# Optimization experiments

Measured on AMD Instinct MI355X. Metric: run time of the kernel, lower is better.

The kernel has to match this reference:

```python
import jax, jax.numpy as jnp
import numpy as np

REL_DIM = 1024
NUM_HEADS = 16
HEAD_DIM = REL_DIM // NUM_HEADS
REL_EMB_DIM = 256
B, K = 32, 512
SCALE = 1.0 / float(np.sqrt(HEAD_DIM))


def setup_inputs() -> dict:
    key = jax.random.key(0)
    ks = jax.random.split(key, 7)
    s = 1.0 / float(np.sqrt(REL_DIM))
    return {
        "h_R": jax.random.normal(ks[0], (B, K, REL_DIM), dtype=jnp.float32),
        "R": jax.random.normal(ks[1], (K, REL_EMB_DIM), dtype=jnp.float32),
        "W_q": jax.random.normal(ks[2], (REL_DIM, REL_DIM), dtype=jnp.float32) * s,
        "W_k": jax.random.normal(ks[3], (REL_DIM, REL_DIM), dtype=jnp.float32) * s,
        "W_v": jax.random.normal(ks[4], (REL_DIM, REL_DIM), dtype=jnp.float32) * s,
        "W_o": jax.random.normal(ks[5], (REL_DIM, REL_DIM), dtype=jnp.float32) * s,
        "w_sim": jax.random.normal(ks[6], (NUM_HEADS,), dtype=jnp.float32) * 0.1,
    }


def reference(h_R, R, W_q, W_k, W_v, W_o, w_sim):
    Bb, Kk, _ = h_R.shape
    H, D = NUM_HEADS, HEAD_DIM
    # torch Linear: x @ W.T ; then split heads -> (B, H, K, D)
    def proj(x, W):
        return jnp.einsum('bkd,ed->bke', x, W).reshape(Bb, Kk, H, D).transpose(0, 2, 1, 3)
    q = proj(h_R, W_q)
    k = proj(h_R, W_k)
    v = proj(h_R, W_v)
    attn = jnp.einsum('bhqd,bhkd->bhqk', q, k) * SCALE
    # cosine-similarity bias (batch-independent): (H, K, K)
    R_norm = R / jnp.maximum(jnp.linalg.norm(R, axis=-1, keepdims=True), 1e-12)
    sim = R_norm @ R_norm.T  # (K, K)
    bias = w_sim[:, None, None] * sim[None]  # (H, K, K)
    attn = attn + bias[None]
    alpha = jax.nn.softmax(attn, axis=-1)
    out = jnp.einsum('bhqk,bhkd->bhqd', alpha, v)
    out = out.transpose(0, 2, 1, 3).reshape(Bb, Kk, H * D)
    return jnp.einsum('bkd,ed->bke', out, W_o)
```

## Files before the change

### kernel.cpp

```cpp
#include <hip/hip_runtime.h>

#define SEQK 512
#define NH 16
#define HD 64
#define RD 1024
#define BBATCH 32
#define QK_SCALE 0.125f

typedef unsigned short u16;
using bf16x8 = __attribute__((ext_vector_type(8))) short;
using f32x4  = __attribute__((ext_vector_type(4))) float;

__device__ __forceinline__ u16 f2bf(float f) {
  unsigned u = __float_as_uint(f);
  u += 0x7FFFu + ((u >> 16) & 1u);
  return (u16)(u >> 16);
}
__device__ __forceinline__ float bf2f(u16 v) {
  return __uint_as_float(((unsigned)v) << 16);
}

__device__ __forceinline__ void async_cp16(const void* g, void* l) {
  __builtin_amdgcn_global_load_lds(
      (__attribute__((address_space(1))) void*)(void*)g,
      (__attribute__((address_space(3))) void*)l,
      16, 0, 0);
}

__global__ void convert_kernel(const float* __restrict__ hR,
                               const float* __restrict__ Wq, const float* __restrict__ Wk,
                               const float* __restrict__ Wv, const float* __restrict__ Wo,
                               u16* __restrict__ hR16,
                               u16* __restrict__ Wq16, u16* __restrict__ Wk16,
                               u16* __restrict__ Wv16, u16* __restrict__ Wo16) {
  size_t i4 = (size_t)blockIdx.x * blockDim.x + threadIdx.x;
  size_t e = i4 * 4;
  const float* src; u16* dst; size_t off;
  if (e < 16777216u) { src = hR; dst = hR16; off = e; }
  else {
    size_t r = e - 16777216u;
    int w = (int)(r >> 20);
    off = r & 1048575u;
    src = (w == 0 ? Wq : w == 1 ? Wk : w == 2 ? Wv : Wo);
    dst = (w == 0 ? Wq16 : w == 1 ? Wk16 : w == 2 ? Wv16 : Wo16);
  }
  float4 v = *(const float4*)(src + off);
  ushort4 o;
  o.x = f2bf(v.x); o.y = f2bf(v.y); o.z = f2bf(v.z); o.w = f2bf(v.w);
  *(ushort4*)(dst + off) = o;
}

__global__ void rnorm_kernel(const float* __restrict__ R, float* __restrict__ Rn) {
  int row = blockIdx.x;
  int lane = threadIdx.x;
  float4 v = *(const float4*)(R + (size_t)row * 256 + lane * 4);
  float ss = v.x * v.x + v.y * v.y + v.z * v.z + v.w * v.w;
  for (int off = 32; off; off >>= 1) ss += __shfl_xor(ss, off);
  float s = 1.0f / fmaxf(sqrtf(ss), 1e-12f);
  float4 o = {v.x * s, v.y * s, v.z * s, v.w * s};
  *(float4*)(Rn + (size_t)row * 256 + lane * 4) = o;
}

__global__ void sim_kernel(const float* __restrict__ Rn, u16* __restrict__ sim16) {
  __shared__ float Rl[16 * 256];
  int i0 = blockIdx.x * 16;
  int t = threadIdx.x;
  #pragma unroll
  for (int i = 0; i < 4; i++) {
    int f = t + i * 256;
    *(float4*)&Rl[f * 4] = *(const float4*)(Rn + (size_t)i0 * 256 + f * 4);
  }
  __syncthreads();
  for (int jj = 0; jj < 2; jj++) {
    int j = jj * 256 + t;
    float acc[16];
    #pragma unroll
    for (int i = 0; i < 16; i++) acc[i] = 0.f;
    for (int c = 0; c < 64; c++) {
      float4 rv = *(const float4*)(Rn + (size_t)j * 256 + c * 4);
      #pragma unroll
      for (int i = 0; i < 16; i++) {
        float4 a = *(const float4*)&Rl[i * 256 + c * 4];
        acc[i] += a.x * rv.x + a.y * rv.y + a.z * rv.z + a.w * rv.w;
      }
    }
    #pragma unroll
    for (int i = 0; i < 16; i++) sim16[(size_t)(i0 + i) * 512 + j] = f2bf(acc[i]);
  }
}

template <int MODE>
__global__ __launch_bounds__(256)
void gemm_kernel(const u16* __restrict__ A,
                 const u16* __restrict__ B0, const u16* __restrict__ B1,
                 const u16* __restrict__ B2,
                 u16* __restrict__ q16, u16* __restrict__ k16, u16* __restrict__ v16,
                 float* __restrict__ outF) {
  __shared__ u16 Alds[128 * 32];
  __shared__ u16 Blds[128 * 32];
  int tid = threadIdx.x;
  int wave = tid >> 6, lane = tid & 63;
  int wm = wave & 1, wn = wave >> 1;
  int lr = lane & 15, qd = lane >> 4;
  int mb = blockIdx.x * 128;
  int ny = blockIdx.y;

  const u16* Bmat;
  int nbmat;
  if (MODE == 0) {
    int wsel = ny >> 3;
    Bmat = (wsel == 0 ? B0 : wsel == 1 ? B1 : B2);
    nbmat = (ny & 7) * 128;
  } else {
    Bmat = B0;
    nbmat = ny * 128;
  }

  f32x4 zero = {0.f, 0.f, 0.f, 0.f};
  f32x4 acc[4][4];
  #pragma unroll
  for (int i = 0; i < 4; i++)
    #pragma unroll
    for (int j = 0; j < 4; j++) acc[i][j] = zero;

  for (int kb = 0; kb < 1024; kb += 32) {
    #pragma unroll
    for (int j = 0; j < 2; j++) {
      int r = (wave * 2 + j) * 16 + (lane >> 2);
      int c = (lane & 3) ^ ((r >> 1) & 3);
      async_cp16(A + (size_t)(mb + r) * 1024 + kb + c * 8,
                 &Alds[(wave * 2 + j) * 512]);
      async_cp16(Bmat + (size_t)(nbmat + r) * 1024 + kb + c * 8,
                 &Blds[(wave * 2 + j) * 512]);
    }
    __syncthreads();

    bf16x8 af[4], bf[4];
    #pragma unroll
    for (int mi = 0; mi < 4; mi++) {
      int ra = wm * 64 + mi * 16 + lr;
      af[mi] = *(const bf16x8*)&Alds[ra * 32 + ((qd ^ ((ra >> 1) & 3)) << 3)];
      int rb = wn * 64 + mi * 16 + lr;
      bf[mi] = *(const bf16x8*)&Blds[rb * 32 + ((qd ^ ((rb >> 1) & 3)) << 3)];
    }
    #pragma unroll
    for (int mi = 0; mi < 4; mi++)
      #pragma unroll
      for (int ni = 0; ni < 4; ni++)
        acc[mi][ni] = __builtin_amdgcn_mfma_f32_16x16x32_bf16(af[mi], bf[ni],
                                                              acc[mi][ni], 0, 0, 0);
    __syncthreads();
  }

  if (MODE == 0) {
    int wsel = ny >> 3;
    u16* dst = (wsel == 0 ? q16 : wsel == 1 ? k16 : v16);
    float scl = (wsel == 0) ? QK_SCALE : 1.0f;
    #pragma unroll
    for (int mi = 0; mi < 4; mi++) {
      int m = mb + wm * 64 + mi * 16 + qd * 4;
      int b = m >> 9, kk = m & 511;
      #pragma unroll
      for (int ni = 0; ni < 4; ni++) {
        int n = nbmat + wn * 64 + ni * 16 + lr;
        int h = n >> 6, d = n & 63;
        u16* p = dst + ((size_t)(b * 16 + h) * 512 + kk) * 64 + d;
        #pragma unroll
        for (int r = 0; r < 4; r++) p[(size_t)r * 64] = f2bf(acc[mi][ni][r] * scl);
      }
    }
  } else {
    #pragma unroll
    for (int mi = 0; mi < 4; mi++) {
      int m = mb + wm * 64 + mi * 16 + qd * 4;
      #pragma unroll
      for (int ni = 0; ni < 4; ni++) {
        int n = ny * 128 + wn * 64 + ni * 16 + lr;
        #pragma unroll
        for (int r = 0; r < 4; r++) outF[(size_t)(m + r) * 1024 + n] = acc[mi][ni][r];
      }
    }
  }
}

__global__ void vtrans_kernel(const u16* __restrict__ v16, u16* __restrict__ vt16) {
  __shared__ u16 tile[64 * 72];
  int kt = blockIdx.x;
  int bh = blockIdx.y;
  int t = threadIdx.x;
  const u16* src = v16 + ((size_t)bh * 512 + kt * 64) * 64;
  #pragma unroll
  for (int j = 0; j < 2; j++) {
    int linear = j * 2048 + t * 8;
    int kr = linear >> 6, d0 = linear & 63;
    bf16x8 vv = *(const bf16x8*)(src + (size_t)kr * 64 + d0);
    #pragma unroll
    for (int e = 0; e < 8; e++) tile[kr * 72 + d0 + e] = (u16)vv[e];
  }
  __syncthreads();
  #pragma unroll
  for (int j = 0; j < 2; j++) {
    int linear = j * 2048 + t * 8;
    int dr = linear >> 6, k0 = linear & 63;
    bf16x8 ov;
    #pragma unroll
    for (int e = 0; e < 8; e++) ov[e] = (short)tile[(k0 + e) * 72 + dr];
    *(bf16x8*)(vt16 + ((size_t)bh * 64 + dr) * 512 + kt * 64 + k0) = ov;
  }
}

__global__ __launch_bounds__(256, 3)
void attn_kernel(const u16* __restrict__ q16, const u16* __restrict__ k16,
                 const u16* __restrict__ vt16, const u16* __restrict__ sim16,
                 const float* __restrict__ wsim, u16* __restrict__ attn16) {
  __shared__ u16 Kbuf[128 * 64];
  __shared__ u16 Vbuf[64 * 128];
  __shared__ u16 Plds[4 * 16 * 128];

  int id = blockIdx.x;
  int xcd = id & 7;
  int j = id >> 3;
  int qt = j & 7;
  int bh = xcd * 64 + (j >> 3);
  int b = bh >> 4, h = bh & 15;

  int tid = threadIdx.x;
  int wave = tid >> 6, lane = tid & 63;
  int lr = lane & 15, qd = lane >> 4;
  int qrb = qt * 64 + wave * 16;
  u16* Pw = &Plds[wave * 2048];

  const u16* qp = q16 + ((size_t)bh * 512 + qrb + lr) * 64 + qd * 8;
  bf16x8 aq0 = *(const bf16x8*)qp;
  bf16x8 aq1 = *(const bf16x8*)(qp + 32);

  float ws = wsim[h];
  int row0 = qrb + qd * 4;

  f32x4 zero = {0.f, 0.f, 0.f, 0.f};
  f32x4 o[4];
  #pragma unroll
  for (int nt = 0; nt < 4; nt++) o[nt] = zero;
  float m_run[4] = {-1e30f, -1e30f, -1e30f, -1e30f};
  float l_run[4] = {0.f, 0.f, 0.f, 0.f};

  const u16* kbase = k16 + (size_t)bh * 512 * 64;
  const u16* vbase = vt16 + (size_t)bh * 64 * 512;

  for (int ck = 0; ck < 4; ck++) {
    int k0 = ck * 128;
    __syncthreads();
    #pragma unroll
    for (int jj = 0; jj < 4; jj++) {
      int rbase = wave * 32 + jj * 8;
      int r = rbase + (lane >> 3);
      int c = (lane & 7) ^ (r & 7);
      async_cp16(kbase + (size_t)(k0 + r) * 64 + c * 8, &Kbuf[rbase * 64]);
    }
    #pragma unroll
    for (int jj = 0; jj < 4; jj++) {
      int dbase = wave * 16 + jj * 4;
      int d = dbase + (lane >> 4);
      int c = (lane & 15) ^ (d & 15);
      async_cp16(vbase + (size_t)d * 512 + k0 + c * 8, &Vbuf[dbase * 128]);
    }
    __syncthreads();

    f32x4 s[8];
    #pragma unroll
    for (int jt = 0; jt < 8; jt++) {
      int kl = jt * 16 + lr;
      ushort4 b4 = *(const ushort4*)(sim16 + (size_t)(k0 + kl) * 512 + row0);
      f32x4 t = {ws * bf2f(b4.x), ws * bf2f(b4.y), ws * bf2f(b4.z), ws * bf2f(b4.w)};
      const u16* krow = &Kbuf[kl * 64];
      int sw = kl & 7;
      bf16x8 kf0 = *(const bf16x8*)(krow + ((qd ^ sw) << 3));
      bf16x8 kf1 = *(const bf16x8*)(krow + (((qd + 4) ^ sw) << 3));
      t = __builtin_amdgcn_mfma_f32_16x16x32_bf16(aq0, kf0, t, 0, 0, 0);
      t = __builtin_amdgcn_mfma_f32_16x16x32_bf16(aq1, kf1, t, 0, 0, 0);
      s[jt] = t;
    }
    float mnew[4], alpha[4], csum[4];
    #pragma unroll
    for (int r = 0; r < 4; r++) {
      float m = s[0][r];
      #pragma unroll
      for (int jt = 1; jt < 8; jt++) m = fmaxf(m, s[jt][r]);
      m = fmaxf(m, __shfl_xor(m, 1));
      m = fmaxf(m, __shfl_xor(m, 2));
      m = fmaxf(m, __shfl_xor(m, 4));
      m = fmaxf(m, __shfl_xor(m, 8));
      mnew[r] = fmaxf(m_run[r], m);
      alpha[r] = __expf(m_run[r] - mnew[r]);
      m_run[r] = mnew[r];
      csum[r] = 0.f;
    }
    #pragma unroll
    for (int jt = 0; jt < 8; jt++)
      #pragma unroll
      for (int r = 0; r < 4; r++) {
        float e = __expf(s[jt][r] - mnew[r]);
        s[jt][r] = e;
        csum[r] += e;
      }
    #pragma unroll
    for (int r = 0; r < 4; r++) {
      float t = csum[r];
      t += __shfl_xor(t, 1); t += __shfl_xor(t, 2);
      t += __shfl_xor(t, 4); t += __shfl_xor(t, 8);
      l_run[r] = l_run[r] * alpha[r] + t;
    }
    #pragma unroll
    for (int jt = 0; jt < 8; jt++) {
      int c = jt * 2 + (lr >> 3);
      int e = lr & 7;
      #pragma unroll
      for (int r = 0; r < 4; r++) {
        int row = qd * 4 + r;
        Pw[row * 128 + ((c ^ row) & 15) * 8 + e] = f2bf(s[jt][r]);
      }
    }
    #pragma unroll
    for (int nt = 0; nt < 4; nt++)
      #pragma unroll
      for (int r = 0; r < 4; r++) o[nt][r] *= alpha[r];
    #pragma unroll
    for (int ks = 0; ks < 4; ks++) {
      bf16x8 ap = *(const bf16x8*)&Pw[lr * 128 + (((ks * 4 + qd) ^ lr) & 15) * 8];
      #pragma unroll
      for (int nt = 0; nt < 4; nt++) {
        int d = nt * 16 + lr;
        bf16x8 vf = *(const bf16x8*)&Vbuf[d * 128 + (((ks * 4 + qd) ^ (d & 15)) << 3)];
        o[nt] = __builtin_amdgcn_mfma_f32_16x16x32_bf16(ap, vf, o[nt], 0, 0, 0);
      }
    }
  }

  float inv[4];
  #pragma unroll
  for (int r = 0; r < 4; r++) inv[r] = 1.0f / l_run[r];
  u16* Ow = Pw;
  #pragma unroll
  for (int nt = 0; nt < 4; nt++)
    #pragma unroll
    for (int r = 0; r < 4; r++)
      Ow[(qd * 4 + r) * 72 + nt * 16 + lr] = f2bf(o[nt][r] * inv[r]);
  #pragma unroll
  for (int it = 0; it < 2; it++) {
    int row = it * 8 + (lane >> 3);
    int seg = lane & 7;
    bf16x8 val = *(const bf16x8*)&Ow[row * 72 + seg * 8];
    *(bf16x8*)(attn16 + ((size_t)b * 512 + qrb + row) * 1024 + h * 64 + seg * 8) = val;
  }
}

extern "C" void kernel_launch(void* const* d_in, const int* in_sizes, int n_in,
                              void* d_out, int out_size, void* d_ws, size_t ws_size,
                              hipStream_t stream) {
  const float* hR  = (const float*)d_in[0];
  const float* R   = (const float*)d_in[1];
  const float* Wq  = (const float*)d_in[2];
  const float* Wk  = (const float*)d_in[3];
  const float* Wv  = (const float*)d_in[4];
  const float* Wo  = (const float*)d_in[5];
  const float* wsm = (const float*)d_in[6];
  float* out = (float*)d_out;

  const size_t NE = 16777216;
  u16* ws16   = (u16*)d_ws;
  u16* hR16   = ws16;
  u16* attn16 = ws16;
  u16* q16    = ws16 + NE;
  u16* k16    = ws16 + 2 * NE;
  u16* v16    = ws16 + 3 * NE;
  u16* vt16   = ws16 + 4 * NE;
  u16* Wq16   = ws16 + 5 * NE;
  u16* Wk16   = Wq16 + 1048576;
  u16* Wv16   = Wk16 + 1048576;
  u16* Wo16   = Wv16 + 1048576;
  u16* sim16  = Wo16 + 1048576;
  float* Rn   = (float*)(sim16 + 262144);

  convert_kernel<<<20480, 256, 0, stream>>>(hR, Wq, Wk, Wv, Wo,
                                            hR16, Wq16, Wk16, Wv16, Wo16);
  rnorm_kernel<<<512, 64, 0, stream>>>(R, Rn);
  sim_kernel<<<32, 256, 0, stream>>>(Rn, sim16);
  gemm_kernel<0><<<dim3(128, 24), 256, 0, stream>>>(hR16, Wq16, Wk16, Wv16,
                                                    q16, k16, v16, nullptr);
  vtrans_kernel<<<dim3(8, 512), 256, 0, stream>>>(v16, vt16);
  attn_kernel<<<4096, 256, 0, stream>>>(q16, k16, vt16, sim16, wsm, attn16);
  gemm_kernel<1><<<dim3(128, 8), 256, 0, stream>>>(attn16, Wo16, nullptr, nullptr,
                                                   nullptr, nullptr, nullptr, out);
}
```

Before: 499.0 us.

## Double-buffer K/V tiles in attention and switch softmax to base-2 exp

Gives the attention kernel two LDS buffers for K and V. The next 128-key chunk is fetched asynchronously while the current chunk is computed, leaving one barrier per iteration instead of two. The log2(e) factor is folded into the Q projection scale and the similarity-bias weight, so the softmax can use a raw v_exp_f32 (exp2) instead of __expf. The larger LDS footprint lowers the launch-bound occupancy hint from 3 to 2 blocks per CU, which may reduce latency hiding.

```diff
diff --git a/kernel.cpp b/kernel.cpp
--- a/kernel.cpp
+++ b/kernel.cpp
@@ -6,6 +6,7 @@
 #define RD 1024
 #define BBATCH 32
 #define QK_SCALE 0.125f
+#define LOG2E 1.4426950408889634f
 
 typedef unsigned short u16;
 using bf16x8 = __attribute__((ext_vector_type(8))) short;
@@ -18,6 +19,11 @@
 }
 __device__ __forceinline__ float bf2f(u16 v) {
   return __uint_as_float(((unsigned)v) << 16);
+}
+__device__ __forceinline__ float fexp2(float x) {
+  float r;
+  asm("v_exp_f32 %0, %1" : "=v"(r) : "v"(x));
+  return r;
 }
 
 __device__ __forceinline__ void async_cp16(const void* g, void* l) {
@@ -155,7 +161,7 @@
   if (MODE == 0) {
     int wsel = ny >> 3;
     u16* dst = (wsel == 0 ? q16 : wsel == 1 ? k16 : v16);
-    float scl = (wsel == 0) ? QK_SCALE : 1.0f;
+    float scl = (wsel == 0) ? QK_SCALE * LOG2E : 1.0f;
     #pragma unroll
     for (int mi = 0; mi < 4; mi++) {
       int m = mb + wm * 64 + mi * 16 + qd * 4;
@@ -209,12 +215,12 @@
   }
 }
 
-__global__ __launch_bounds__(256, 3)
+__global__ __launch_bounds__(256, 2)
 void attn_kernel(const u16* __restrict__ q16, const u16* __restrict__ k16,
                  const u16* __restrict__ vt16, const u16* __restrict__ sim16,
                  const float* __restrict__ wsim, u16* __restrict__ attn16) {
-  __shared__ u16 Kbuf[128 * 64];
-  __shared__ u16 Vbuf[64 * 128];
+  __shared__ u16 Kbuf[2][128 * 64];
+  __shared__ u16 Vbuf[2][64 * 128];
   __shared__ u16 Plds[4 * 16 * 128];
 
   int id = blockIdx.x;
@@ -234,7 +240,7 @@
   bf16x8 aq0 = *(const bf16x8*)qp;
   bf16x8 aq1 = *(const bf16x8*)(qp + 32);
 
-  float ws = wsim[h];
+  float ws = wsim[h] * LOG2E;
   int row0 = qrb + qd * 4;
 
   f32x4 zero = {0.f, 0.f, 0.f, 0.f};
@@ -247,24 +253,33 @@
   const u16* kbase = k16 + (size_t)bh * 512 * 64;
   const u16* vbase = vt16 + (size_t)bh * 64 * 512;
 
-  for (int ck = 0; ck < 4; ck++) {
+  auto stage = [&](int nb, int ck) {
     int k0 = ck * 128;
-    __syncthreads();
     #pragma unroll
     for (int jj = 0; jj < 4; jj++) {
       int rbase = wave * 32 + jj * 8;
       int r = rbase + (lane >> 3);
       int c = (lane & 7) ^ (r & 7);
-      async_cp16(kbase + (size_t)(k0 + r) * 64 + c * 8, &Kbuf[rbase * 64]);
+      async_cp16(kbase + (size_t)(k0 + r) * 64 + c * 8, &Kbuf[nb][rbase * 64]);
     }
     #pragma unroll
     for (int jj = 0; jj < 4; jj++) {
       int dbase = wave * 16 + jj * 4;
       int d = dbase + (lane >> 4);
       int c = (lane & 15) ^ (d & 15);
-      async_cp16(vbase + (size_t)d * 512 + k0 + c * 8, &Vbuf[dbase * 128]);
-    }
-    __syncthreads();
+      async_cp16(vbase + (size_t)d * 512 + k0 + c * 8, &Vbuf[nb][dbase * 128]);
+    }
+  };
+
+  stage(0, 0);
+  __syncthreads();
+
+  int cb = 0;
+  for (int ck = 0; ck < 4; ck++) {
+    if (ck < 3) stage(cb ^ 1, ck + 1);
+    int k0 = ck * 128;
+    const u16* Kc = &Kbuf[cb][0];
+    const u16* Vc = &Vbuf[cb][0];
 
     f32x4 s[8];
     #pragma unroll
@@ -272,7 +287,7 @@
       int kl = jt * 16 + lr;
       ushort4 b4 = *(const ushort4*)(sim16 + (size_t)(k0 + kl) * 512 + row0);
       f32x4 t = {ws * bf2f(b4.x), ws * bf2f(b4.y), ws * bf2f(b4.z), ws * bf2f(b4.w)};
-      const u16* krow = &Kbuf[kl * 64];
+      const u16* krow = Kc + kl * 64;
       int sw = kl & 7;
       bf16x8 kf0 = *(const bf16x8*)(krow + ((qd ^ sw) << 3));
       bf16x8 kf1 = *(const bf16x8*)(krow + (((qd + 4) ^ sw) << 3));
@@ -291,7 +306,7 @@
       m = fmaxf(m, __shfl_xor(m, 4));
       m = fmaxf(m, __shfl_xor(m, 8));
       mnew[r] = fmaxf(m_run[r], m);
-      alpha[r] = __expf(m_run[r] - mnew[r]);
+      alpha[r] = fexp2(m_run[r] - mnew[r]);
       m_run[r] = mnew[r];
       csum[r] = 0.f;
     }
@@ -299,7 +314,7 @@
     for (int jt = 0; jt < 8; jt++)
       #pragma unroll
       for (int r = 0; r < 4; r++) {
-        float e = __expf(s[jt][r] - mnew[r]);
+        float e = fexp2(s[jt][r] - mnew[r]);
         s[jt][r] = e;
         csum[r] += e;
       }
@@ -330,10 +345,12 @@
       #pragma unroll
       for (int nt = 0; nt < 4; nt++) {
         int d = nt * 16 + lr;
-        bf16x8 vf = *(const bf16x8*)&Vbuf[d * 128 + (((ks * 4 + qd) ^ (d & 15)) << 3)];
+        bf16x8 vf = *(const bf16x8*)&Vc[d * 128 + (((ks * 4 + qd) ^ (d & 15)) << 3)];
         o[nt] = __builtin_amdgcn_mfma_f32_16x16x32_bf16(ap, vf, o[nt], 0, 0, 0);
       }
     }
+    if (ck < 3) __syncthreads();
+    cb ^= 1;
   }
 
   float inv[4];
```

New measurement: 506.7 us. Within noise of the previous version (+1.5%).
